# Kernel tuning notes

Hardware: AMD Instinct MI355X
Metric: run time of the kernel (lower is better)

Reference implementation:

```python
import jax, jax.numpy as jnp
import numpy as np

B, S, H, R = 64, 2048, 512, 256
NEG = -1.0e9


def setup_inputs() -> dict:
    key = jax.random.key(0)
    ks = jax.random.split(key, 12)
    sc_h = 1.0 / np.sqrt(H)
    sc_r = 1.0 / np.sqrt(R)
    return {
        "sent_h": jax.random.normal(ks[0], (B, S, H), jnp.float32),
        "rel": jax.random.normal(ks[1], (B, R), jnp.float32),
        "pool": jax.random.normal(ks[2], (B, H), jnp.float32),
        "mask": jax.random.randint(ks[3], (B, S), 0, 2, jnp.int32),
        "Wg_w": jax.random.normal(ks[4], (H, H), jnp.float32) * sc_h,
        "Wg_b": jnp.zeros((H,), jnp.float32),
        "Wh_w": jax.random.normal(ks[5], (H, H), jnp.float32) * sc_h,
        "Wh_b": jnp.zeros((H,), jnp.float32),
        "Wr_w": jax.random.normal(ks[6], (H, R), jnp.float32) * sc_r,
        "Wr_b": jnp.zeros((H,), jnp.float32),
        "alpha_w": jax.random.normal(ks[7], (1, H), jnp.float32) * sc_h,
        "alpha_b": jnp.zeros((1,), jnp.float32),
    }


def reference(sent_h, rel, pool, mask, Wg_w, Wg_b, Wh_w, Wh_b, Wr_w, Wr_b, alpha_w, alpha_b):
    # linear projections (torch Linear: x @ W.T + b)
    relation = rel @ Wr_w.T + Wr_b          # [B, H]
    sent = jnp.einsum('bsh,kh->bsk', sent_h, Wh_w) + Wh_b  # [B, S, H]
    global_sen = pool @ Wg_w.T + Wg_b       # [B, H]
    mix = jnp.tanh(relation[:, None, :] + sent + global_sen[:, None, :])  # [B, S, H]
    weight = jnp.einsum('bsh,h->bs', mix, alpha_w[0]) + alpha_b[0]        # [B, S]
    weight = jnp.where(mask == 0, NEG, weight)
    weight_ = jax.nn.softmax(weight, axis=-1)
    att_res = jnp.einsum('bs,bsh->bh', weight_, sent)  # [B, H]
    return (att_res, weight_)
```

## Files before the change

### kernel.cpp

```cpp
#include <hip/hip_runtime.h>
#include <cstdint>
#include <cstddef>

#define B_ 64
#define S_ 2048
#define H_ 512
#define R_ 256
#define M_ (B_ * S_)
#define NEGV (-1.0e9f)

typedef short short8 __attribute__((ext_vector_type(8)));
typedef unsigned short u16x8 __attribute__((ext_vector_type(8)));
typedef float f32x4 __attribute__((ext_vector_type(4)));
typedef unsigned short u16;

__device__ __forceinline__ u16 f2b(float x) {
    union { float f; uint32_t u; } c; c.f = x;
    uint32_t u = c.u;
    uint32_t r = (u + 0x7fffu + ((u >> 16) & 1u)) >> 16;
    return (u16)r;
}
__device__ __forceinline__ float b2f(u16 u) {
    union { uint32_t u; float f; } c; c.u = ((uint32_t)u) << 16;
    return c.f;
}
__device__ __forceinline__ float fast_tanh(float v) {
    float e = __expf(2.0f * v);
    return 1.0f - 2.0f / (e + 1.0f);
}
__device__ __forceinline__ void load_lds16(const void* g, void* l) {
    __builtin_amdgcn_global_load_lds((__attribute__((address_space(1))) void*)g,
                                     (__attribute__((address_space(3))) void*)l,
                                     16, 0, 0);
}

__global__ void k_convert(const float* __restrict__ sent, u16* __restrict__ sentb) {
    const long n8 = (long)M_ * H_ / 8;
    long stride = (long)gridDim.x * blockDim.x;
    for (long i = (long)blockIdx.x * blockDim.x + threadIdx.x; i < n8; i += stride) {
        float4 v0 = ((const float4*)sent)[2 * i];
        float4 v1 = ((const float4*)sent)[2 * i + 1];
        u16x8 o;
        o[0] = f2b(v0.x); o[1] = f2b(v0.y); o[2] = f2b(v0.z); o[3] = f2b(v0.w);
        o[4] = f2b(v1.x); o[5] = f2b(v1.y); o[6] = f2b(v1.z); o[7] = f2b(v1.w);
        ((u16x8*)sentb)[i] = o;
    }
}

__global__ void k_base(const float* __restrict__ rel, const float* __restrict__ pool,
                       const float* __restrict__ Wg_w, const float* __restrict__ Wg_b,
                       const float* __restrict__ Wh_b,
                       const float* __restrict__ Wr_w, const float* __restrict__ Wr_b,
                       const float* __restrict__ whw, float* __restrict__ base,
                       u16* __restrict__ whwb) {
    int tid = threadIdx.x;
    {
        int gi = blockIdx.x * 256 + tid;
        float4 v = ((const float4*)whw)[gi];
        ushort4 o; o.x = f2b(v.x); o.y = f2b(v.y); o.z = f2b(v.z); o.w = f2b(v.w);
        ((ushort4*)whwb)[gi] = o;
    }
    int b = blockIdx.x >> 2, q = blockIdx.x & 3;
    __shared__ __attribute__((aligned(16))) float srel[R_];
    __shared__ __attribute__((aligned(16))) float spool[H_];
    __shared__ float accs[128];
    srel[tid & 255] = rel[b * R_ + (tid & 255)];
    for (int i = tid; i < H_; i += 256) spool[i] = pool[b * H_ + i];
    __syncthreads();
    int kk = tid & 127, half = tid >> 7;
    int k = q * 128 + kk;
    float acc = 0.f;
    if (half == 0) {
        acc = Wr_b[k] + Wg_b[k] + Wh_b[k];
        const float4* wr = (const float4*)(Wr_w + (size_t)k * R_);
        #pragma unroll 8
        for (int r4 = 0; r4 < R_ / 4; ++r4) {
            float4 w = wr[r4]; float4 x = ((const float4*)srel)[r4];
            acc += w.x * x.x + w.y * x.y + w.z * x.z + w.w * x.w;
        }
        const float4* wg = (const float4*)(Wg_w + (size_t)k * H_);
        #pragma unroll 8
        for (int h4 = 0; h4 < 32; ++h4) {
            float4 w = wg[h4]; float4 x = ((const float4*)spool)[h4];
            acc += w.x * x.x + w.y * x.y + w.z * x.z + w.w * x.w;
        }
    } else {
        const float4* wg = (const float4*)(Wg_w + (size_t)k * H_);
        #pragma unroll 8
        for (int h4 = 32; h4 < 128; ++h4) {
            float4 w = wg[h4]; float4 x = ((const float4*)spool)[h4];
            acc += w.x * x.x + w.y * x.y + w.z * x.z + w.w * x.w;
        }
    }
    if (half) accs[kk] = acc;
    __syncthreads();
    if (!half) base[b * H_ + k] = acc + accs[kk];
}

__launch_bounds__(256)
__global__ void k_gemm(const u16* __restrict__ A,
                       const u16* __restrict__ Bw,
                       const float* __restrict__ base,
                       const float* __restrict__ alpha,
                       float* __restrict__ partial)
{
    const int K = 512;
    int j = blockIdx.x;
    int xcd  = j & 7;
    int slot = j >> 3;
    int nb   = slot & 3;
    int mb   = (slot >> 2) * 8 + xcd;
    int m0 = mb * 128;
    int n0 = nb * 128;
    int b  = m0 >> 11;

    int tid = threadIdx.x;
    int w  = tid >> 6;
    int l  = tid & 63;
    int wm = w & 1, wn = w >> 1;
    int lr = l & 15;
    int lq = l >> 4;

    __shared__ u16 smA[128 * 64];
    __shared__ u16 smB[128 * 64];
    __shared__ float red[2][2][64];

    f32x4 zero = {0.f, 0.f, 0.f, 0.f};
    f32x4 acc[4][4];
    #pragma unroll
    for (int i = 0; i < 4; ++i)
        #pragma unroll
        for (int jj = 0; jj < 4; ++jj) acc[i][jj] = zero;

    for (int kt = 0; kt < 8; ++kt) {
        int k0 = kt * 64;
        #pragma unroll
        for (int i = 0; i < 4; ++i) {
            int c  = w * 4 + i;
            int mf = c >> 1, kc = c & 1;
            int row = mf * 16 + lr;
            int col = k0 + kc * 32 + lq * 8;
            const u16* ga = A  + (size_t)(m0 + row) * K + col;
            const u16* gb = Bw + (size_t)(n0 + row) * K + col;
            load_lds16(ga, smA + c * 512);
            load_lds16(gb, smB + c * 512);
        }
        __syncthreads();
        #pragma unroll
        for (int kc = 0; kc < 2; ++kc) {
            short8 af[4], bf[4];
            #pragma unroll
            for (int mi = 0; mi < 4; ++mi)
                af[mi] = *(const short8*)(smA + ((wm * 4 + mi) * 2 + kc) * 512 + l * 8);
            #pragma unroll
            for (int ni = 0; ni < 4; ++ni)
                bf[ni] = *(const short8*)(smB + ((wn * 4 + ni) * 2 + kc) * 512 + l * 8);
            #pragma unroll
            for (int mi = 0; mi < 4; ++mi)
                #pragma unroll
                for (int ni = 0; ni < 4; ++ni)
                    acc[mi][ni] = __builtin_amdgcn_mfma_f32_16x16x32_bf16(af[mi], bf[ni], acc[mi][ni], 0, 0, 0);
        }
        __syncthreads();
    }

    float basev[4], alphav[4];
    #pragma unroll
    for (int ni = 0; ni < 4; ++ni) {
        int n = n0 + wn * 64 + ni * 16 + lr;
        basev[ni]  = base[b * H_ + n];
        alphav[ni] = alpha[n];
    }
    #pragma unroll
    for (int mi = 0; mi < 4; ++mi) {
        #pragma unroll
        for (int r = 0; r < 4; ++r) {
            float s = 0.f;
            #pragma unroll
            for (int ni = 0; ni < 4; ++ni) {
                float v = acc[mi][ni][r] + basev[ni];
                s += fast_tanh(v) * alphav[ni];
            }
            s += __shfl_xor(s, 1);
            s += __shfl_xor(s, 2);
            s += __shfl_xor(s, 4);
            s += __shfl_xor(s, 8);
            if (lr == 0) red[wm][wn][mi * 16 + lq * 4 + r] = s;
        }
    }
    __syncthreads();
    if (tid < 128) {
        int wmi = tid >> 6, row = tid & 63;
        float sum = red[wmi][0][row] + red[wmi][1][row];
        partial[(size_t)nb * M_ + m0 + wmi * 64 + row] = sum;
    }
}

__global__ void k_softmax(const float* __restrict__ partial, const int* __restrict__ mask,
                          const float* __restrict__ alpha_b, float* __restrict__ wout) {
    int b = blockIdx.x;
    int tid = threadIdx.x;
    __shared__ float sred[8];
    float x[8];
    float ab = alpha_b[0];
    float lmax = -3.0e38f;
    #pragma unroll
    for (int jj = 0; jj < 8; ++jj) {
        int s = tid + jj * 256;
        size_t m = (size_t)b * S_ + s;
        float v = partial[m] + partial[(size_t)M_ + m] + partial[2 * (size_t)M_ + m] + partial[3 * (size_t)M_ + m] + ab;
        if (mask[b * S_ + s] == 0) v = NEGV;
        x[jj] = v;
        lmax = fmaxf(lmax, v);
    }
    #pragma unroll
    for (int off = 1; off < 64; off <<= 1) lmax = fmaxf(lmax, __shfl_xor(lmax, off));
    int wv = tid >> 6, l = tid & 63;
    if (l == 0) sred[wv] = lmax;
    __syncthreads();
    float gmax = fmaxf(fmaxf(sred[0], sred[1]), fmaxf(sred[2], sred[3]));
    float lsum = 0.f;
    #pragma unroll
    for (int jj = 0; jj < 8; ++jj) { x[jj] = __expf(x[jj] - gmax); lsum += x[jj]; }
    #pragma unroll
    for (int off = 1; off < 64; off <<= 1) lsum += __shfl_xor(lsum, off);
    if (l == 0) sred[4 + wv] = lsum;
    __syncthreads();
    float inv = 1.f / (sred[4] + sred[5] + sred[6] + sred[7]);
    #pragma unroll
    for (int jj = 0; jj < 8; ++jj) {
        int s = tid + jj * 256;
        wout[(size_t)b * S_ + s] = x[jj] * inv;
    }
}

__global__ void k_wsum(const u16* __restrict__ sentb, const float* __restrict__ wrow_g,
                       float* __restrict__ t) {
    int b  = blockIdx.x >> 3;
    int hc = blockIdx.x & 7;
    int tid = threadIdx.x;
    __shared__ __attribute__((aligned(16))) float wrow[S_];
    __shared__ float4 red4[256];
    ((float4*)wrow)[tid]       = ((const float4*)(wrow_g + (size_t)b * S_))[tid];
    ((float4*)wrow)[tid + 256] = ((const float4*)(wrow_g + (size_t)b * S_))[tid + 256];
    __syncthreads();
    int hi = tid & 15, sg = tid >> 4;
    const u16* bp = sentb + (size_t)b * S_ * H_ + hc * 64 + hi * 4;
    float a0 = 0.f, a1 = 0.f, a2 = 0.f, a3 = 0.f;
    for (int s0 = sg; s0 < S_; s0 += 64) {
        #pragma unroll
        for (int u = 0; u < 4; ++u) {
            int s = s0 + u * 16;
            ushort4 v = *(const ushort4*)(bp + (size_t)s * H_);
            float wgt = wrow[s];
            a0 += wgt * b2f(v.x); a1 += wgt * b2f(v.y); a2 += wgt * b2f(v.z); a3 += wgt * b2f(v.w);
        }
    }
    red4[tid] = make_float4(a0, a1, a2, a3);
    __syncthreads();
    if (tid < 16) {
        float4 sacc = red4[tid];
        #pragma unroll
        for (int g = 1; g < 16; ++g) {
            float4 o = red4[g * 16 + tid];
            sacc.x += o.x; sacc.y += o.y; sacc.z += o.z; sacc.w += o.w;
        }
        float* tp = t + (size_t)b * H_ + hc * 64 + tid * 4;
        tp[0] = sacc.x; tp[1] = sacc.y; tp[2] = sacc.z; tp[3] = sacc.w;
    }
}

__global__ void k_att(const float* __restrict__ t, const float* __restrict__ Whw,
                      const float* __restrict__ Whb, float* __restrict__ out) {
    int tid = threadIdx.x;
    int b = blockIdx.x >> 2, q = blockIdx.x & 3;
    __shared__ __attribute__((aligned(16))) float st[H_];
    __shared__ float accs[128];
    for (int i = tid; i < H_; i += 256) st[i] = t[(size_t)b * H_ + i];
    __syncthreads();
    int hh = tid & 127, half = tid >> 7;
    int h = q * 128 + hh;
    const float4* wr = (const float4*)(Whw + (size_t)h * H_) + half * 64;
    const float4* sx = (const float4*)st + half * 64;
    float acc = 0.f;
    #pragma unroll 8
    for (int i = 0; i < 64; ++i) {
        float4 w = wr[i]; float4 x = sx[i];
        acc += w.x * x.x + w.y * x.y + w.z * x.z + w.w * x.w;
    }
    if (half) accs[hh] = acc;
    __syncthreads();
    if (!half) out[(size_t)b * H_ + h] = acc + accs[hh] + Whb[h];
}

extern "C" void kernel_launch(void* const* d_in, const int* in_sizes, int n_in,
                              void* d_out, int out_size, void* d_ws, size_t ws_size,
                              hipStream_t stream) {
    const float* sent_h  = (const float*)d_in[0];
    const float* rel     = (const float*)d_in[1];
    const float* pool    = (const float*)d_in[2];
    const int*   mask    = (const int*)d_in[3];
    const float* Wg_w    = (const float*)d_in[4];
    const float* Wg_b    = (const float*)d_in[5];
    const float* Wh_w    = (const float*)d_in[6];
    const float* Wh_b    = (const float*)d_in[7];
    const float* Wr_w    = (const float*)d_in[8];
    const float* Wr_b    = (const float*)d_in[9];
    const float* alpha_w = (const float*)d_in[10];
    const float* alpha_b = (const float*)d_in[11];
    float* out = (float*)d_out;

    char* ws = (char*)d_ws;
    u16*   sentb   = (u16*)ws;
    u16*   whwb    = (u16*)(ws + 134217728);
    float* base    = (float*)(ws + 134217728 + 524288);
    float* partial = (float*)(ws + 134217728 + 524288 + 131072);
    float* tbuf    = (float*)(ws + 134217728 + 524288 + 131072 + 2097152);

    float* att_out = out;
    float* w_out   = out + B_ * H_;

    k_convert<<<dim3(4096), dim3(256), 0, stream>>>(sent_h, sentb);
    k_base<<<dim3(256), dim3(256), 0, stream>>>(rel, pool, Wg_w, Wg_b, Wh_b, Wr_w, Wr_b, Wh_w, base, whwb);
    k_gemm<<<dim3((M_ / 128) * 4), dim3(256), 0, stream>>>(sentb, whwb, base, alpha_w, partial);
    k_softmax<<<dim3(B_), dim3(256), 0, stream>>>(partial, mask, alpha_b, w_out);
    k_wsum<<<dim3(B_ * 8), dim3(256), 0, stream>>>(sentb, w_out, tbuf);
    k_att<<<dim3(256), dim3(256), 0, stream>>>(tbuf, Wh_w, Wh_b, att_out);
}
```

Baseline: 614.4 us.

## Double-buffer LDS tiles in score GEMM and streamline tanh epilogue

The score GEMM now uses two LDS buffers and prefetches the next K-tile via global_load_lds while MFMAs run on the current one, removing one barrier per iteration. MFMA sections are wrapped in s_setprio to favour the math waves. The tanh·alpha epilogue is rewritten algebraically to use a single fma, a hardware exp2 and a hardware rcp per element, folding the constant term into an initial sum. This doubles LDS usage to 64KB per block, which may reduce occupancy, and the rcp approximation slightly changes precision.

```diff
diff --git a/kernel.cpp b/kernel.cpp
--- a/kernel.cpp
+++ b/kernel.cpp
@@ -23,10 +23,6 @@
 __device__ __forceinline__ float b2f(u16 u) {
     union { uint32_t u; float f; } c; c.u = ((uint32_t)u) << 16;
     return c.f;
-}
-__device__ __forceinline__ float fast_tanh(float v) {
-    float e = __expf(2.0f * v);
-    return 1.0f - 2.0f / (e + 1.0f);
 }
 __device__ __forceinline__ void load_lds16(const void* g, void* l) {
     __builtin_amdgcn_global_load_lds((__attribute__((address_space(1))) void*)g,
@@ -121,8 +117,8 @@
     int lr = l & 15;
     int lq = l >> 4;
 
-    __shared__ u16 smA[128 * 64];
-    __shared__ u16 smB[128 * 64];
+    __shared__ __attribute__((aligned(16))) u16 smA[2][128 * 64];
+    __shared__ __attribute__((aligned(16))) u16 smB[2][128 * 64];
     __shared__ float red[2][2][64];
 
     f32x4 zero = {0.f, 0.f, 0.f, 0.f};
@@ -132,7 +128,7 @@
         #pragma unroll
         for (int jj = 0; jj < 4; ++jj) acc[i][jj] = zero;
 
-    for (int kt = 0; kt < 8; ++kt) {
+    auto STAGE = [&](int buf, int kt) {
         int k0 = kt * 64;
         #pragma unroll
         for (int i = 0; i < 4; ++i) {
@@ -142,44 +138,60 @@
             int col = k0 + kc * 32 + lq * 8;
             const u16* ga = A  + (size_t)(m0 + row) * K + col;
             const u16* gb = Bw + (size_t)(n0 + row) * K + col;
-            load_lds16(ga, smA + c * 512);
-            load_lds16(gb, smB + c * 512);
-        }
-        __syncthreads();
+            load_lds16(ga, smA[buf] + c * 512);
+            load_lds16(gb, smB[buf] + c * 512);
+        }
+    };
+
+    STAGE(0, 0);
+    __syncthreads();
+
+    #pragma unroll
+    for (int kt = 0; kt < 8; ++kt) {
+        int cur = kt & 1;
+        if (kt < 7) STAGE(cur ^ 1, kt + 1);
+        __builtin_amdgcn_s_setprio(1);
         #pragma unroll
         for (int kc = 0; kc < 2; ++kc) {
             short8 af[4], bf[4];
             #pragma unroll
             for (int mi = 0; mi < 4; ++mi)
-                af[mi] = *(const short8*)(smA + ((wm * 4 + mi) * 2 + kc) * 512 + l * 8);
+                af[mi] = *(const short8*)(smA[cur] + ((wm * 4 + mi) * 2 + kc) * 512 + l * 8);
             #pragma unroll
             for (int ni = 0; ni < 4; ++ni)
-                bf[ni] = *(const short8*)(smB + ((wn * 4 + ni) * 2 + kc) * 512 + l * 8);
+                bf[ni] = *(const short8*)(smB[cur] + ((wn * 4 + ni) * 2 + kc) * 512 + l * 8);
             #pragma unroll
             for (int mi = 0; mi < 4; ++mi)
                 #pragma unroll
                 for (int ni = 0; ni < 4; ++ni)
                     acc[mi][ni] = __builtin_amdgcn_mfma_f32_16x16x32_bf16(af[mi], bf[ni], acc[mi][ni], 0, 0, 0);
         }
+        __builtin_amdgcn_s_setprio(0);
         __syncthreads();
     }
 
-    float basev[4], alphav[4];
+    const float C2 = 2.8853900817779268f;
+    float base2[4], a2[4];
+    float asum = 0.f;
     #pragma unroll
     for (int ni = 0; ni < 4; ++ni) {
         int n = n0 + wn * 64 + ni * 16 + lr;
-        basev[ni]  = base[b * H_ + n];
-        alphav[ni] = alpha[n];
+        base2[ni] = C2 * base[b * H_ + n];
+        float al  = alpha[n];
+        a2[ni] = 2.0f * al;
+        asum  += al;
     }
     #pragma unroll
     for (int mi = 0; mi < 4; ++mi) {
         #pragma unroll
         for (int r = 0; r < 4; ++r) {
-            float s = 0.f;
+            float s = asum;
             #pragma unroll
             for (int ni = 0; ni < 4; ++ni) {
-                float v = acc[mi][ni][r] + basev[ni];
-                s += fast_tanh(v) * alphav[ni];
+                float f  = fmaf(acc[mi][ni][r], C2, base2[ni]);
+                float e  = __builtin_amdgcn_exp2f(f);
+                float rr = __builtin_amdgcn_rcpf(e + 1.0f);
+                s = fmaf(-a2[ni], rr, s);
             }
             s += __shfl_xor(s, 1);
             s += __shfl_xor(s, 2);
```

After: 598.4 us. 1.03x faster.
